# Kernel tuning notes

Measured on AMD Instinct MI355X. Metric: run time of the kernel, lower is better.

## Reference

```python
import jax, jax.numpy as jnp
import numpy as np

D_MODEL = 768
NHEAD = 12
DK = D_MODEL // NHEAD
MAX_DIST = 1000.0
FF = 3072
POS_HIDDEN = 32  # hidden width of the relative-position bias MLP
EPS = 1e-5
B, L = 2, 1024


def setup_inputs() -> dict:
    key = jax.random.key(0)
    ks = jax.random.split(key, 24)

    def lin(k, i, o):  # torch-Linear-like init, stored as (in, out)
        return jax.random.uniform(k, (i, o), jnp.float32, -1.0, 1.0) / np.sqrt(i)

    return {
        "src": jax.random.normal(ks[0], (B, L, D_MODEL), jnp.float32),
        "src_x": jax.random.uniform(ks[1], (B, L), jnp.float32) * 1000.0,
        "src_y": jax.random.uniform(ks[2], (B, L), jnp.float32) * 1000.0,
        # attention projections (q,k,v,out)
        "Wq": lin(ks[3], D_MODEL, D_MODEL), "bq": jnp.zeros((D_MODEL,), jnp.float32),
        "Wk": lin(ks[4], D_MODEL, D_MODEL), "bk": jnp.zeros((D_MODEL,), jnp.float32),
        "Wv": lin(ks[5], D_MODEL, D_MODEL), "bv": jnp.zeros((D_MODEL,), jnp.float32),
        "Wo": lin(ks[6], D_MODEL, D_MODEL), "bo": jnp.zeros((D_MODEL,), jnp.float32),
        # relative-position bias MLP: 2 -> POS_HIDDEN -> NHEAD
        "P1": lin(ks[7], 2, POS_HIDDEN), "pb1": jnp.zeros((POS_HIDDEN,), jnp.float32),
        "P2": lin(ks[8], POS_HIDDEN, NHEAD), "pb2": jnp.zeros((NHEAD,), jnp.float32),
        # FFN
        "W1": lin(ks[9], D_MODEL, FF), "b1": jnp.zeros((FF,), jnp.float32),
        "W2": lin(ks[10], FF, D_MODEL), "b2": jnp.zeros((D_MODEL,), jnp.float32),
        # post-LN params
        "g1": jnp.ones((D_MODEL,), jnp.float32), "be1": jnp.zeros((D_MODEL,), jnp.float32),
        "g2": jnp.ones((D_MODEL,), jnp.float32), "be2": jnp.zeros((D_MODEL,), jnp.float32),
    }


def _layernorm(x, g, b):
    m = jnp.mean(x, axis=-1, keepdims=True)
    v = jnp.var(x, axis=-1, keepdims=True)
    return (x - m) * jax.lax.rsqrt(v + EPS) * g + b


def reference(src, src_x, src_y, Wq, bq, Wk, bk, Wv, bv, Wo, bo,
              P1, pb1, P2, pb2, W1, b1, W2, b2, g1, be1, g2, be2):
    b, l, _ = src.shape
    # projections -> (b, h, l, dk)
    q = (src @ Wq + bq).reshape(b, l, NHEAD, DK).transpose(0, 2, 1, 3)
    k = (src @ Wk + bk).reshape(b, l, NHEAD, DK).transpose(0, 2, 1, 3)
    v = (src @ Wv + bv).reshape(b, l, NHEAD, DK).transpose(0, 2, 1, 3)
    # 2D relative positions, clipped and normalized to [-1, 1]
    rx = jnp.clip(src_x[:, :, None] - src_x[:, None, :], -MAX_DIST, MAX_DIST) / MAX_DIST
    ry = jnp.clip(src_y[:, :, None] - src_y[:, None, :], -MAX_DIST, MAX_DIST) / MAX_DIST
    rel = jnp.stack([rx, ry], axis=-1)                        # (b, l, l, 2)
    bias = jax.nn.relu(rel @ P1 + pb1) @ P2 + pb2             # (b, l, l, h)
    bias = bias.transpose(0, 3, 1, 2)                         # (b, h, l, l)
    scores = jnp.einsum('bhqd,bhkd->bhqk', q, k) / np.sqrt(DK).astype(np.float32) + bias
    attn = jax.nn.softmax(scores, axis=-1)
    o = jnp.einsum('bhqk,bhkd->bhqd', attn, v).transpose(0, 2, 1, 3).reshape(b, l, D_MODEL)
    src2 = o @ Wo + bo
    x = _layernorm(src + src2, g1, be1)                       # post-LN residual 1
    ff = jax.nn.relu(x @ W1 + b1) @ W2 + b2                   # FFN
    return _layernorm(x + ff, g2, be2)                        # post-LN residual 2
```

## Files before the change

kernel.cpp:

```cpp
#include <hip/hip_runtime.h>
#include <math.h>

typedef unsigned short ushort_t;
typedef __attribute__((ext_vector_type(8))) short bf16x8;
typedef __attribute__((ext_vector_type(4))) float f32x4;

constexpr int kD      = 768;
constexpr int kNH     = 12;
constexpr int kDK     = 64;
constexpr int kFF     = 3072;
constexpr int kL      = 1024;
constexpr int kRows   = 2048;
constexpr float kEPS  = 1e-5f;

__device__ __forceinline__ ushort_t f2bf(float f) {
    union { float f; unsigned u; } v; v.f = f;
    unsigned r = (v.u + 0x7fffu + ((v.u >> 16) & 1u)) >> 16;
    return (ushort_t)r;
}
__device__ __forceinline__ float bf2f(ushort_t u) {
    union { unsigned u; float f; } v; v.u = ((unsigned)u) << 16; return v.f;
}

#define GL_LDS(gp, lp) __builtin_amdgcn_global_load_lds( \
    (const __attribute__((address_space(1))) void*)(gp), \
    (__attribute__((address_space(3))) void*)(lp), 16, 0, 0)

template<int RELU, int OUTBF, int ADDBIAS>
__device__ __forceinline__ void gemm_body(const ushort_t* __restrict__ A,
                                          const ushort_t* __restrict__ WT,
                                          const float* __restrict__ bias,
                                          void* __restrict__ Cout,
                                          int N, int K, int row0, int col0,
                                          int kbeg, int kend)
{
    __shared__ ushort_t lds[8192];
    ushort_t* As = lds;
    ushort_t* Bs = lds + 4096;

    const int tid  = threadIdx.x;
    const int lane = tid & 63;
    const int wave = tid >> 6;
    const int wrow = (wave & 1) * 64;
    const int wcol = (wave >> 1) * 64;

    const int srow = wave * 16 + (lane >> 2);
    const int sk   = (lane & 3) * 8;
    const ushort_t* ga0 = A  + (size_t)(row0 + srow)      * K + sk;
    const ushort_t* ga1 = A  + (size_t)(row0 + srow + 64) * K + sk;
    const ushort_t* gb0 = WT + (size_t)(col0 + srow)      * K + sk;
    const ushort_t* gb1 = WT + (size_t)(col0 + srow + 64) * K + sk;
    ushort_t* la0 = As + wave * 512;
    ushort_t* la1 = As + 2048 + wave * 512;
    ushort_t* lb0 = Bs + wave * 512;
    ushort_t* lb1 = Bs + 2048 + wave * 512;

    const int fl = lane & 15, fq = lane >> 4;
    const ushort_t* fa[4];
    const ushort_t* fb[4];
    #pragma unroll
    for (int i = 0; i < 4; ++i) {
        fa[i] = As + (wrow + i * 16 + fl) * 32 + fq * 8;
        fb[i] = Bs + (wcol + i * 16 + fl) * 32 + fq * 8;
    }

    f32x4 acc[4][4] = {};

    for (int k0 = kbeg; k0 < kend; k0 += 32) {
        __syncthreads();
        GL_LDS(ga0 + k0, la0);
        GL_LDS(ga1 + k0, la1);
        GL_LDS(gb0 + k0, lb0);
        GL_LDS(gb1 + k0, lb1);
        __syncthreads();

        bf16x8 av[4], bv[4];
        #pragma unroll
        for (int i = 0; i < 4; ++i) {
            av[i] = *(const bf16x8*)fa[i];
            bv[i] = *(const bf16x8*)fb[i];
        }
        #pragma unroll
        for (int mi = 0; mi < 4; ++mi)
            #pragma unroll
            for (int ni = 0; ni < 4; ++ni)
                acc[mi][ni] = __builtin_amdgcn_mfma_f32_16x16x32_bf16(
                    av[mi], bv[ni], acc[mi][ni], 0, 0, 0);
    }

    #pragma unroll
    for (int mi = 0; mi < 4; ++mi) {
        const int m = wrow + mi * 16 + fq * 4;
        #pragma unroll
        for (int ni = 0; ni < 4; ++ni) {
            const int n = wcol + ni * 16 + fl;
            const float bb = ADDBIAS ? bias[col0 + n] : 0.f;
            #pragma unroll
            for (int r = 0; r < 4; ++r) {
                float v = acc[mi][ni][r] + bb;
                if (RELU) v = fmaxf(v, 0.f);
                const size_t idx = (size_t)(row0 + m + r) * N + col0 + n;
                if (OUTBF) ((ushort_t*)Cout)[idx] = f2bf(v);
                else       ((float*)Cout)[idx]    = v;
            }
        }
    }
}

template<int RELU, int OUTBF>
__global__ __launch_bounds__(256)
void gemm_kernel(const ushort_t* __restrict__ A, const ushort_t* __restrict__ WT,
                 const float* __restrict__ bias, void* __restrict__ Cout,
                 int N, int K)
{
    gemm_body<RELU, OUTBF, 1>(A, WT, bias, Cout, N, K,
                              blockIdx.y * 128, blockIdx.x * 128, 0, K);
}

__global__ __launch_bounds__(256)
void gemm_splitk_kernel(const ushort_t* __restrict__ A, const ushort_t* __restrict__ WT,
                        float* __restrict__ parts, int N, int K, int kslice)
{
    const int z = blockIdx.z;
    float* out = parts + (size_t)z * kRows * N;
    gemm_body<0, 0, 0>(A, WT, nullptr, out, N, K,
                       blockIdx.y * 128, blockIdx.x * 128, z * kslice, (z + 1) * kslice);
}

__global__ __launch_bounds__(256)
void gemm_qkv_kernel(const ushort_t* __restrict__ A,
                     const ushort_t* wq, const ushort_t* wk, const ushort_t* wv,
                     const float* bq, const float* bk, const float* bv,
                     ushort_t* q, ushort_t* k, ushort_t* v)
{
    const ushort_t* WT; const float* bias; ushort_t* out;
    if (blockIdx.z == 0)      { WT = wq; bias = bq; out = q; }
    else if (blockIdx.z == 1) { WT = wk; bias = bk; out = k; }
    else                      { WT = wv; bias = bv; out = v; }
    gemm_body<0, 1, 1>(A, WT, bias, out, kD, kD,
                       blockIdx.y * 128, blockIdx.x * 128, 0, kD);
}

struct WtDesc { const float* src; ushort_t* dst; int K; int N; };
struct WtArgs { WtDesc d[3]; };

__global__ __launch_bounds__(256)
void wt_kernel(WtArgs args)
{
    const WtDesc w = args.d[blockIdx.z];
    const int ktiles = w.K >> 6;
    const int kt = (blockIdx.x % ktiles) * 64;
    const int nt = (blockIdx.x / ktiles) * 64;
    if (nt >= w.N) return;

    __shared__ float T[64][65];
    const int tid = threadIdx.x;
    #pragma unroll
    for (int i = 0; i < 4; ++i) {
        const int e = tid + i * 256;
        const int r = e >> 4;
        const int c = (e & 15) * 4;
        const float4 f = *(const float4*)&w.src[(size_t)(kt + r) * w.N + nt + c];
        T[c + 0][r] = f.x; T[c + 1][r] = f.y; T[c + 2][r] = f.z; T[c + 3][r] = f.w;
    }
    __syncthreads();
    #pragma unroll
    for (int i = 0; i < 4; ++i) {
        const int e = tid + i * 256;
        const int n = e >> 4;
        const int kc = (e & 15) * 4;
        ushort4 o;
        o.x = f2bf(T[n][kc + 0]); o.y = f2bf(T[n][kc + 1]);
        o.z = f2bf(T[n][kc + 2]); o.w = f2bf(T[n][kc + 3]);
        *(ushort4*)&w.dst[(size_t)(nt + n) * w.K + kt + kc] = o;
    }
}

__global__ __launch_bounds__(256)
void cvt_kernel(const float* __restrict__ in, ushort_t* __restrict__ out, int n4)
{
    const int i = blockIdx.x * 256 + threadIdx.x;
    if (i < n4) {
        const float4 f = ((const float4*)in)[i];
        ushort4 o;
        o.x = f2bf(f.x); o.y = f2bf(f.y); o.z = f2bf(f.z); o.w = f2bf(f.w);
        ((ushort4*)out)[i] = o;
    }
}

__global__ __launch_bounds__(256)
void vtrans_kernel(const ushort_t* __restrict__ vb, ushort_t* __restrict__ vt)
{
    const int bh = blockIdx.x;
    const int b = bh / kNH, h = bh - b * kNH;
    const int j0 = blockIdx.y * 64;
    __shared__ ushort_t T[64][72];

    const int tid = threadIdx.x;
    {
        const int jr = tid & 63;
        const int c0 = (tid >> 6) * 16;
        const ushort_t* sp = vb + (size_t)(b * kL + j0 + jr) * kD + h * kDK + c0;
        uint4 u0 = *(const uint4*)sp;
        uint4 u1 = *(const uint4*)(sp + 8);
        const ushort_t* e0 = (const ushort_t*)&u0;
        const ushort_t* e1 = (const ushort_t*)&u1;
        #pragma unroll
        for (int jj = 0; jj < 8; ++jj) {
            T[c0 + jj][jr]     = e0[jj];
            T[c0 + 8 + jj][jr] = e1[jj];
        }
    }
    __syncthreads();
    {
        const int dr = tid >> 2;
        const int jc = (tid & 3) * 16;
        ushort_t* dp = vt + (size_t)(bh * 64 + dr) * kL + j0 + jc;
        *(uint4*)dp       = *(const uint4*)&T[dr][jc];
        *(uint4*)(dp + 8) = *(const uint4*)&T[dr][jc + 8];
    }
}

__global__ __launch_bounds__(256, 4)
void bias_kernel(const float* __restrict__ sx, const float* __restrict__ sy,
                 const float* __restrict__ P1, const float* __restrict__ pb1,
                 const float* __restrict__ P2, const float* __restrict__ pb2,
                 ushort_t* __restrict__ biasb)
{
    const int bid = blockIdx.x;
    const int b  = bid >> 10;
    const int qt = (bid >> 4) & 63;
    const int kt = bid & 15;
    const int tid = threadIdx.x;

    __shared__ float P[32][16];
    __shared__ float pb2l[12];
    __shared__ float qxl[16], qyl[16], kxl[64], kyl[64];
    __shared__ ushort_t Btile[12 * 1024];

    if (tid < 32) {
        P[tid][0] = P1[tid];
        P[tid][1] = P1[32 + tid];
        P[tid][2] = pb1[tid];
        P[tid][3] = 0.f;
    }
    for (int e = tid; e < 384; e += 256) P[e / 12][4 + e % 12] = P2[e];
    if (tid < 12) pb2l[tid] = pb2[tid];
    if (tid < 16) { qxl[tid] = sx[b * kL + qt * 16 + tid];
                    qyl[tid] = sy[b * kL + qt * 16 + tid]; }
    if (tid < 64) { kxl[tid] = sx[b * kL + kt * 64 + tid];
                    kyl[tid] = sy[b * kL + kt * 64 + tid]; }
    __syncthreads();

    const int ri = tid >> 4;
    const int fl = tid & 15;
    const int fq = ri >> 2, r = ri & 3;
    const int lane16 = fq * 16 + fl;
    const float xi = qxl[ri], yi = qyl[ri];

    float rx[4], ry[4];
    #pragma unroll
    for (int n = 0; n < 4; ++n) {
        const int cj = n * 16 + fl;
        rx[n] = fminf(fmaxf(xi - kxl[cj], -1000.f), 1000.f) * 1e-3f;
        ry[n] = fminf(fmaxf(yi - kyl[cj], -1000.f), 1000.f) * 1e-3f;
    }

    float acc[4][12] = {};
    #pragma unroll 4
    for (int u = 0; u < 32; ++u) {
        const float4 pc = *(const float4*)&P[u][0];
        const float4 w0 = *(const float4*)&P[u][4];
        const float4 w1 = *(const float4*)&P[u][8];
        const float4 w2 = *(const float4*)&P[u][12];
        float t[4];
        #pragma unroll
        for (int n = 0; n < 4; ++n)
            t[n] = fmaxf(fmaf(rx[n], pc.x, fmaf(ry[n], pc.y, pc.z)), 0.f);
        #pragma unroll
        for (int n = 0; n < 4; ++n) {
            acc[n][0]  = fmaf(t[n], w0.x, acc[n][0]);
            acc[n][1]  = fmaf(t[n], w0.y, acc[n][1]);
            acc[n][2]  = fmaf(t[n], w0.z, acc[n][2]);
            acc[n][3]  = fmaf(t[n], w0.w, acc[n][3]);
            acc[n][4]  = fmaf(t[n], w1.x, acc[n][4]);
            acc[n][5]  = fmaf(t[n], w1.y, acc[n][5]);
            acc[n][6]  = fmaf(t[n], w1.z, acc[n][6]);
            acc[n][7]  = fmaf(t[n], w1.w, acc[n][7]);
            acc[n][8]  = fmaf(t[n], w2.x, acc[n][8]);
            acc[n][9]  = fmaf(t[n], w2.y, acc[n][9]);
            acc[n][10] = fmaf(t[n], w2.z, acc[n][10]);
            acc[n][11] = fmaf(t[n], w2.w, acc[n][11]);
        }
    }

    #pragma unroll
    for (int h = 0; h < 12; ++h) {
        const float pb = pb2l[h] - 4.0f;
        #pragma unroll
        for (int n = 0; n < 4; ++n)
            Btile[h * 1024 + lane16 * 16 + n * 4 + r] = f2bf(acc[n][h] + pb);
    }
    __syncthreads();

    #pragma unroll
    for (int i = 0; i < 6; ++i) {
        const int off = (i * 256 + tid) * 8;
        const int h = off >> 10;
        const int inner = off & 1023;
        ushort_t* dst = biasb +
            (((size_t)(b * kNH + h) * 64 + qt) * 16 + kt) * 1024 + inner;
        *(uint4*)dst = *(const uint4*)&Btile[off];
    }
}

__global__ __launch_bounds__(256)
void attn_kernel(const ushort_t* __restrict__ qg, const ushort_t* __restrict__ kg,
                 const ushort_t* __restrict__ vt, const ushort_t* __restrict__ biasb,
                 ushort_t* __restrict__ og)
{
    const int bh = blockIdx.x;
    const int b  = bh / kNH, h = bh - b * kNH;
    const int qt = blockIdx.y;
    const int q0 = qt * 16;
    const int tid = threadIdx.x;
    const int z  = tid >> 6;
    const int lane = tid & 63;
    const int fl = lane & 15, fq = lane >> 4;

    __shared__ ushort_t Sp[4][16][72];
    __shared__ ushort_t Ob[4][16][64];
    __shared__ float    Ll[4][16];

    const size_t qoff = (size_t)(b * kL + q0 + fl) * kD + h * kDK + fq * 8;
    const bf16x8 aq0 = *(const bf16x8*)(qg + qoff);
    const bf16x8 aq1 = *(const bf16x8*)(qg + qoff + 32);

    const ushort_t* kbase = kg + (size_t)(b * kL) * kD + h * kDK + fq * 8;
    const ushort_t* vbase = vt + (size_t)(bh * 64) * kL + fq * 8;
    const ushort_t* btile = biasb +
        ((size_t)(bh * 64 + qt) * 16 + z * 4) * 1024 + lane * 16;

    f32x4 accO[4] = {};
    float l_part[4] = {};

    bf16x8 kc[4][2];
    uint4 bc0, bc1;
    {
        const int k0 = z * 256;
        #pragma unroll
        for (int n = 0; n < 4; ++n) {
            const ushort_t* kr = kbase + (size_t)(k0 + n * 16 + fl) * kD;
            kc[n][0] = *(const bf16x8*)kr;
            kc[n][1] = *(const bf16x8*)(kr + 32);
        }
        bc0 = *(const uint4*)btile;
        bc1 = *(const uint4*)(btile + 8);
    }

    #pragma unroll
    for (int t = 0; t < 4; ++t) {
        const int k0 = z * 256 + t * 64;

        bf16x8 vv[4][2];
        #pragma unroll
        for (int n = 0; n < 4; ++n) {
            const ushort_t* vr = vbase + (size_t)(n * 16 + fl) * kL + k0;
            vv[n][0] = *(const bf16x8*)vr;
            vv[n][1] = *(const bf16x8*)(vr + 32);
        }

        f32x4 S[4] = {};
        #pragma unroll
        for (int n = 0; n < 4; ++n) {
            S[n] = __builtin_amdgcn_mfma_f32_16x16x32_bf16(aq0, kc[n][0], S[n], 0, 0, 0);
            S[n] = __builtin_amdgcn_mfma_f32_16x16x32_bf16(aq1, kc[n][1], S[n], 0, 0, 0);
        }

        bf16x8 kn[4][2];
        uint4 bn0, bn1;
        if (t < 3) {
            #pragma unroll
            for (int n = 0; n < 4; ++n) {
                const ushort_t* kr = kbase + (size_t)(k0 + 64 + n * 16 + fl) * kD;
                kn[n][0] = *(const bf16x8*)kr;
                kn[n][1] = *(const bf16x8*)(kr + 32);
            }
            bn0 = *(const uint4*)(btile + (t + 1) * 1024);
            bn1 = *(const uint4*)(btile + (t + 1) * 1024 + 8);
        }

        ushort_t bu[16];
        *(uint4*)&bu[0] = bc0;
        *(uint4*)&bu[8] = bc1;

        #pragma unroll
        for (int n = 0; n < 4; ++n)
            #pragma unroll
            for (int r = 0; r < 4; ++r) {
                const float e = __expf(fmaf(S[n][r], 0.125f, bf2f(bu[n * 4 + r])));
                S[n][r] = e;
                l_part[r] += e;
            }

        #pragma unroll
        for (int n = 0; n < 4; ++n)
            #pragma unroll
            for (int r = 0; r < 4; ++r)
                Sp[z][fq * 4 + r][n * 16 + fl] = f2bf(S[n][r]);

        const bf16x8 ap0 = *(const bf16x8*)&Sp[z][fl][fq * 8];
        const bf16x8 ap1 = *(const bf16x8*)&Sp[z][fl][32 + fq * 8];
        #pragma unroll
        for (int n = 0; n < 4; ++n) {
            accO[n] = __builtin_amdgcn_mfma_f32_16x16x32_bf16(ap0, vv[n][0], accO[n], 0, 0, 0);
            accO[n] = __builtin_amdgcn_mfma_f32_16x16x32_bf16(ap1, vv[n][1], accO[n], 0, 0, 0);
        }

        if (t < 3) {
            #pragma unroll
            for (int n = 0; n < 4; ++n) { kc[n][0] = kn[n][0]; kc[n][1] = kn[n][1]; }
            bc0 = bn0; bc1 = bn1;
        }
    }

    float l_full[4], inv[4];
    #pragma unroll
    for (int r = 0; r < 4; ++r) {
        float l = l_part[r];
        l += __shfl_xor(l, 1, 16);
        l += __shfl_xor(l, 2, 16);
        l += __shfl_xor(l, 4, 16);
        l += __shfl_xor(l, 8, 16);
        l_full[r] = l;
        inv[r] = 1.0f / l;
    }

    #pragma unroll
    for (int n = 0; n < 4; ++n)
        #pragma unroll
        for (int r = 0; r < 4; ++r)
            Ob[z][fq * 4 + r][n * 16 + fl] = f2bf(accO[n][r] * inv[r]);
    if (fl == 0) {
        #pragma unroll
        for (int r = 0; r < 4; ++r)
            Ll[z][fq * 4 + r] = l_full[r];
    }
    __syncthreads();

    {
        const int ri = tid >> 4;
        const int d0 = (tid & 15) * 4;
        const float w0 = Ll[0][ri], w1 = Ll[1][ri], w2 = Ll[2][ri], w3 = Ll[3][ri];
        const float winv = 1.0f / (w0 + w1 + w2 + w3);
        const float c0 = w0 * winv, c1 = w1 * winv, c2 = w2 * winv, c3 = w3 * winv;

        ushort_t o[4];
        #pragma unroll
        for (int j = 0; j < 4; ++j)
            o[j] = f2bf(fmaf(c0, bf2f(Ob[0][ri][d0 + j]),
                        fmaf(c1, bf2f(Ob[1][ri][d0 + j]),
                        fmaf(c2, bf2f(Ob[2][ri][d0 + j]),
                             c3 * bf2f(Ob[3][ri][d0 + j])))));
        *(uint2*)&og[(size_t)(b * kL + q0 + ri) * kD + h * kDK + d0] = *(const uint2*)o;
    }
}

template<int NPART, int DUAL>
__global__ __launch_bounds__(256)
void ln_kernel(const float* __restrict__ a, const float* __restrict__ parts,
               const float* __restrict__ bias,
               const float* __restrict__ g, const float* __restrict__ be,
               float* __restrict__ out, ushort_t* __restrict__ out_bf)
{
    const int row = blockIdx.x;
    const int tid = threadIdx.x;
    const float* pa = a + (size_t)row * kD;
    constexpr size_t NTOK = (size_t)kRows * kD;

    float v[3];
    float s = 0.f, sq = 0.f;
    #pragma unroll
    for (int i = 0; i < 3; ++i) {
        const int d = tid + i * 256;
        float t = pa[d] + bias[d];
        #pragma unroll
        for (int p = 0; p < NPART; ++p)
            t += parts[p * NTOK + (size_t)row * kD + d];
        v[i] = t;
        s  += t;
        sq += t * t;
    }
    #pragma unroll
    for (int off = 32; off > 0; off >>= 1) {
        s  += __shfl_down(s, off);
        sq += __shfl_down(sq, off);
    }
    __shared__ float bs[4], bq2[4];
    if ((tid & 63) == 0) { bs[tid >> 6] = s; bq2[tid >> 6] = sq; }
    __syncthreads();
    const float ts = bs[0] + bs[1] + bs[2] + bs[3];
    const float tq = bq2[0] + bq2[1] + bq2[2] + bq2[3];
    const float invn = 1.0f / (float)kD;
    const float mean = ts * invn;
    const float var  = tq * invn - mean * mean;
    const float rstd = rsqrtf(var + kEPS);

    float* po = out + (size_t)row * kD;
    #pragma unroll
    for (int i = 0; i < 3; ++i) {
        const int d = tid + i * 256;
        const float o = (v[i] - mean) * rstd * g[d] + be[d];
        po[d] = o;
        if (DUAL) out_bf[(size_t)row * kD + d] = f2bf(o);
    }
}

extern "C" void kernel_launch(void* const* d_in, const int* in_sizes, int n_in,
                              void* d_out, int out_size, void* d_ws, size_t ws_size,
                              hipStream_t stream)
{
    const float* src = (const float*)d_in[0];
    const float* sx  = (const float*)d_in[1];
    const float* sy  = (const float*)d_in[2];
    const float* Wq  = (const float*)d_in[3];  const float* bq  = (const float*)d_in[4];
    const float* Wk  = (const float*)d_in[5];  const float* bk  = (const float*)d_in[6];
    const float* Wv  = (const float*)d_in[7];  const float* bv  = (const float*)d_in[8];
    const float* Wo  = (const float*)d_in[9];  const float* bo  = (const float*)d_in[10];
    const float* P1  = (const float*)d_in[11]; const float* pb1 = (const float*)d_in[12];
    const float* P2  = (const float*)d_in[13]; const float* pb2 = (const float*)d_in[14];
    const float* W1  = (const float*)d_in[15]; const float* b1  = (const float*)d_in[16];
    const float* W2  = (const float*)d_in[17]; const float* b2  = (const float*)d_in[18];
    const float* g1  = (const float*)d_in[19]; const float* be1 = (const float*)d_in[20];
    const float* g2  = (const float*)d_in[21]; const float* be2 = (const float*)d_in[22];

    constexpr size_t W768  = 768u * 768u;
    constexpr size_t W3072 = 768u * 3072u;
    constexpr size_t NTOK  = (size_t)kRows * kD;

    ushort_t* wsu = (ushort_t*)d_ws;
    ushort_t* wqT = wsu;
    ushort_t* wkT = wqT + W768;
    ushort_t* wvT = wkT + W768;
    ushort_t* qb  = wvT + W768;
    ushort_t* kb  = qb + NTOK;
    ushort_t* vb  = kb + NTOK;
    ushort_t* sb  = vb + NTOK;
    ushort_t* vtb = sb + NTOK;
    ushort_t* biasb = vtb + NTOK;
    ushort_t* woT   = biasb;
    ushort_t* w1T   = woT + W768;
    ushort_t* w2T   = w1T + W3072;
    float*    xb    = (float*)(w2T + W3072);
    ushort_t* h1bf  = (ushort_t*)(xb + NTOK);
    float*    s2p   = (float*)h1bf;
    float*    ff2p  = (float*)(h1bf + 4 * NTOK);
    ushort_t* xbf   = qb;

    const dim3 blk(256);

    WtArgs wa_early;
    wa_early.d[0] = { Wq, wqT, kD, kD };
    wa_early.d[1] = { Wk, wkT, kD, kD };
    wa_early.d[2] = { Wv, wvT, kD, kD };
    wt_kernel<<<dim3(144, 1, 3), blk, 0, stream>>>(wa_early);
    cvt_kernel<<<dim3((int)(NTOK / 4 / 256)), blk, 0, stream>>>(src, sb, (int)(NTOK / 4));
    bias_kernel<<<dim3(2048), blk, 0, stream>>>(sx, sy, P1, pb1, P2, pb2, biasb);

    gemm_qkv_kernel<<<dim3(kD / 128, kRows / 128, 3), blk, 0, stream>>>(
        sb, wqT, wkT, wvT, bq, bk, bv, qb, kb, vb);

    vtrans_kernel<<<dim3(2 * kNH, kL / 64), blk, 0, stream>>>(vb, vtb);

    attn_kernel<<<dim3(2 * kNH, kL / 16), blk, 0, stream>>>(qb, kb, vtb, biasb, sb);

    WtArgs wa_late;
    wa_late.d[0] = { Wo, woT, kD,  kD  };
    wa_late.d[1] = { W1, w1T, kD,  kFF };
    wa_late.d[2] = { W2, w2T, kFF, kD  };
    wt_kernel<<<dim3(576, 1, 3), blk, 0, stream>>>(wa_late);

    gemm_splitk_kernel<<<dim3(kD / 128, kRows / 128, 2), blk, 0, stream>>>(
        sb, woT, s2p, kD, kD, kD / 2);

    ln_kernel<2, 1><<<dim3(kRows), blk, 0, stream>>>(src, s2p, bo, g1, be1, xb, xbf);

    gemm_kernel<1, 1><<<dim3(kFF / 128, kRows / 128), blk, 0, stream>>>(
        xbf, w1T, b1, h1bf, kFF, kD);

    gemm_splitk_kernel<<<dim3(kD / 128, kRows / 128, 3), blk, 0, stream>>>(
        h1bf, w2T, ff2p, kD, kFF, kFF / 3);

    ln_kernel<3, 0><<<dim3(kRows), blk, 0, stream>>>(xb, ff2p, b2, g2, be2,
                                                     (float*)d_out, nullptr);
}
```

Measured before the change: 300.8 us.

## Merge independent kernels into combined launches to cut launch count and gaps

Three pairs of independent work now share one launch each, dispatched by block index: the Wq/Wk/Wv weight transposes with the src bf16 conversion, the QKV GEMM with the position-bias MLP, and attention with the late weight transposes (Wo/W1/W2). The late weight copies move to a separate buffer region after the FFN partial sums, since the old woT location overlaps the bias buffer that attention still reads. This removes three kernel launches and lets small jobs fill idle CUs beside heavier ones. In exchange, shared memory per block is sized to the largest branch, which can lower occupancy for the lighter branches, and block scheduling order affects how well the work overlaps.

Result: faster. 290.9 us (-3.3%).

```diff
diff --git a/kernel.cpp b/kernel.cpp
--- a/kernel.cpp
+++ b/kernel.cpp
@@ -32,9 +32,8 @@
                                           const float* __restrict__ bias,
                                           void* __restrict__ Cout,
                                           int N, int K, int row0, int col0,
-                                          int kbeg, int kend)
-{
-    __shared__ ushort_t lds[8192];
+                                          int kbeg, int kend, ushort_t* lds)
+{
     ushort_t* As = lds;
     ushort_t* Bs = lds + 4096;
 
@@ -113,54 +112,34 @@
                  const float* __restrict__ bias, void* __restrict__ Cout,
                  int N, int K)
 {
+    __shared__ ushort_t lds[8192];
     gemm_body<RELU, OUTBF, 1>(A, WT, bias, Cout, N, K,
-                              blockIdx.y * 128, blockIdx.x * 128, 0, K);
+                              blockIdx.y * 128, blockIdx.x * 128, 0, K, lds);
 }
 
 __global__ __launch_bounds__(256)
 void gemm_splitk_kernel(const ushort_t* __restrict__ A, const ushort_t* __restrict__ WT,
                         float* __restrict__ parts, int N, int K, int kslice)
 {
+    __shared__ ushort_t lds[8192];
     const int z = blockIdx.z;
     float* out = parts + (size_t)z * kRows * N;
     gemm_body<0, 0, 0>(A, WT, nullptr, out, N, K,
-                       blockIdx.y * 128, blockIdx.x * 128, z * kslice, (z + 1) * kslice);
-}
-
-__global__ __launch_bounds__(256)
-void gemm_qkv_kernel(const ushort_t* __restrict__ A,
-                     const ushort_t* wq, const ushort_t* wk, const ushort_t* wv,
-                     const float* bq, const float* bk, const float* bv,
-                     ushort_t* q, ushort_t* k, ushort_t* v)
-{
-    const ushort_t* WT; const float* bias; ushort_t* out;
-    if (blockIdx.z == 0)      { WT = wq; bias = bq; out = q; }
-    else if (blockIdx.z == 1) { WT = wk; bias = bk; out = k; }
-    else                      { WT = wv; bias = bv; out = v; }
-    gemm_body<0, 1, 1>(A, WT, bias, out, kD, kD,
-                       blockIdx.y * 128, blockIdx.x * 128, 0, kD);
-}
-
-struct WtDesc { const float* src; ushort_t* dst; int K; int N; };
-struct WtArgs { WtDesc d[3]; };
-
-__global__ __launch_bounds__(256)
-void wt_kernel(WtArgs args)
-{
-    const WtDesc w = args.d[blockIdx.z];
-    const int ktiles = w.K >> 6;
-    const int kt = (blockIdx.x % ktiles) * 64;
-    const int nt = (blockIdx.x / ktiles) * 64;
-    if (nt >= w.N) return;
-
-    __shared__ float T[64][65];
-    const int tid = threadIdx.x;
+                       blockIdx.y * 128, blockIdx.x * 128,
+                       z * kslice, (z + 1) * kslice, lds);
+}
+
+__device__ __forceinline__ void wt_tile(const float* __restrict__ src,
+                                        ushort_t* __restrict__ dst,
+                                        int K, int N, int kt, int nt,
+                                        float (*T)[65], int tid)
+{
     #pragma unroll
     for (int i = 0; i < 4; ++i) {
         const int e = tid + i * 256;
         const int r = e >> 4;
         const int c = (e & 15) * 4;
-        const float4 f = *(const float4*)&w.src[(size_t)(kt + r) * w.N + nt + c];
+        const float4 f = *(const float4*)&src[(size_t)(kt + r) * N + nt + c];
         T[c + 0][r] = f.x; T[c + 1][r] = f.y; T[c + 2][r] = f.z; T[c + 3][r] = f.w;
     }
     __syncthreads();
@@ -172,107 +151,92 @@
         ushort4 o;
         o.x = f2bf(T[n][kc + 0]); o.y = f2bf(T[n][kc + 1]);
         o.z = f2bf(T[n][kc + 2]); o.w = f2bf(T[n][kc + 3]);
-        *(ushort4*)&w.dst[(size_t)(nt + n) * w.K + kt + kc] = o;
+        *(ushort4*)&dst[(size_t)(nt + n) * K + kt + kc] = o;
     }
 }
 
 __global__ __launch_bounds__(256)
-void cvt_kernel(const float* __restrict__ in, ushort_t* __restrict__ out, int n4)
-{
-    const int i = blockIdx.x * 256 + threadIdx.x;
-    if (i < n4) {
-        const float4 f = ((const float4*)in)[i];
+void prep_kernel(const float* __restrict__ Wq, const float* __restrict__ Wk,
+                 const float* __restrict__ Wv,
+                 ushort_t* wqT, ushort_t* wkT, ushort_t* wvT,
+                 const float* __restrict__ src, ushort_t* __restrict__ sb)
+{
+    __shared__ float T[64][65];
+    const int bid = blockIdx.x;
+    const int tid = threadIdx.x;
+
+    if (bid < 432) {
+        const int wz = bid / 144, t = bid - wz * 144;
+        const float* s = (wz == 0) ? Wq : (wz == 1) ? Wk : Wv;
+        ushort_t*   d = (wz == 0) ? wqT : (wz == 1) ? wkT : wvT;
+        wt_tile(s, d, kD, kD, (t % 12) * 64, (t / 12) * 64, T, tid);
+    } else {
+        const int i = (bid - 432) * 256 + tid;
+        const float4 f = ((const float4*)src)[i];
         ushort4 o;
         o.x = f2bf(f.x); o.y = f2bf(f.y); o.z = f2bf(f.z); o.w = f2bf(f.w);
-        ((ushort4*)out)[i] = o;
-    }
-}
-
-__global__ __launch_bounds__(256)
-void vtrans_kernel(const ushort_t* __restrict__ vb, ushort_t* __restrict__ vt)
-{
-    const int bh = blockIdx.x;
-    const int b = bh / kNH, h = bh - b * kNH;
-    const int j0 = blockIdx.y * 64;
-    __shared__ ushort_t T[64][72];
-
-    const int tid = threadIdx.x;
-    {
-        const int jr = tid & 63;
-        const int c0 = (tid >> 6) * 16;
-        const ushort_t* sp = vb + (size_t)(b * kL + j0 + jr) * kD + h * kDK + c0;
-        uint4 u0 = *(const uint4*)sp;
-        uint4 u1 = *(const uint4*)(sp + 8);
-        const ushort_t* e0 = (const ushort_t*)&u0;
-        const ushort_t* e1 = (const ushort_t*)&u1;
-        #pragma unroll
-        for (int jj = 0; jj < 8; ++jj) {
-            T[c0 + jj][jr]     = e0[jj];
-            T[c0 + 8 + jj][jr] = e1[jj];
-        }
-    }
-    __syncthreads();
-    {
-        const int dr = tid >> 2;
-        const int jc = (tid & 3) * 16;
-        ushort_t* dp = vt + (size_t)(bh * 64 + dr) * kL + j0 + jc;
-        *(uint4*)dp       = *(const uint4*)&T[dr][jc];
-        *(uint4*)(dp + 8) = *(const uint4*)&T[dr][jc + 8];
-    }
-}
-
-__global__ __launch_bounds__(256, 4)
-void bias_kernel(const float* __restrict__ sx, const float* __restrict__ sy,
+        ((ushort4*)sb)[i] = o;
+    }
+}
+
+struct BiasSmem {
+    float P[32][16];
+    float pb2l[12];
+    float qxl[16], qyl[16], kxl[64], kyl[64];
+    ushort_t Btile[12 * 1024];
+};
+struct AttnSmem {
+    ushort_t Sp[4][16][72];
+    ushort_t Ob[4][16][64];
+    float    Ll[4][16];
+};
+
+__device__ __forceinline__ void bias_body(int bid, BiasSmem& S,
+                 const float* __restrict__ sx, const float* __restrict__ sy,
                  const float* __restrict__ P1, const float* __restrict__ pb1,
                  const float* __restrict__ P2, const float* __restrict__ pb2,
                  ushort_t* __restrict__ biasb)
 {
-    const int bid = blockIdx.x;
     const int b  = bid >> 10;
     const int qt = (bid >> 4) & 63;
     const int kt = bid & 15;
     const int tid = threadIdx.x;
 
-    __shared__ float P[32][16];
-    __shared__ float pb2l[12];
-    __shared__ float qxl[16], qyl[16], kxl[64], kyl[64];
-    __shared__ ushort_t Btile[12 * 1024];
-
     if (tid < 32) {
-        P[tid][0] = P1[tid];
-        P[tid][1] = P1[32 + tid];
-        P[tid][2] = pb1[tid];
-        P[tid][3] = 0.f;
-    }
-    for (int e = tid; e < 384; e += 256) P[e / 12][4 + e % 12] = P2[e];
-    if (tid < 12) pb2l[tid] = pb2[tid];
-    if (tid < 16) { qxl[tid] = sx[b * kL + qt * 16 + tid];
-                    qyl[tid] = sy[b * kL + qt * 16 + tid]; }
-    if (tid < 64) { kxl[tid] = sx[b * kL + kt * 64 + tid];
-                    kyl[tid] = sy[b * kL + kt * 64 + tid]; }
+        S.P[tid][0] = P1[tid];
+        S.P[tid][1] = P1[32 + tid];
+        S.P[tid][2] = pb1[tid];
+        S.P[tid][3] = 0.f;
+    }
+    for (int e = tid; e < 384; e += 256) S.P[e / 12][4 + e % 12] = P2[e];
+    if (tid < 12) S.pb2l[tid] = pb2[tid];
+    if (tid < 16) { S.qxl[tid] = sx[b * kL + qt * 16 + tid];
+                    S.qyl[tid] = sy[b * kL + qt * 16 + tid]; }
+    if (tid < 64) { S.kxl[tid] = sx[b * kL + kt * 64 + tid];
+                    S.kyl[tid] = sy[b * kL + kt * 64 + tid]; }
     __syncthreads();
 
     const int ri = tid >> 4;
     const int fl = tid & 15;
     const int fq = ri >> 2, r = ri & 3;
     const int lane16 = fq * 16 + fl;
-    const float xi = qxl[ri], yi = qyl[ri];
+    const float xi = S.qxl[ri], yi = S.qyl[ri];
 
     float rx[4], ry[4];
     #pragma unroll
     for (int n = 0; n < 4; ++n) {
         const int cj = n * 16 + fl;
-        rx[n] = fminf(fmaxf(xi - kxl[cj], -1000.f), 1000.f) * 1e-3f;
-        ry[n] = fminf(fmaxf(yi - kyl[cj], -1000.f), 1000.f) * 1e-3f;
+        rx[n] = fminf(fmaxf(xi - S.kxl[cj], -1000.f), 1000.f) * 1e-3f;
+        ry[n] = fminf(fmaxf(yi - S.kyl[cj], -1000.f), 1000.f) * 1e-3f;
     }
 
     float acc[4][12] = {};
     #pragma unroll 4
     for (int u = 0; u < 32; ++u) {
-        const float4 pc = *(const float4*)&P[u][0];
-        const float4 w0 = *(const float4*)&P[u][4];
-        const float4 w1 = *(const float4*)&P[u][8];
-        const float4 w2 = *(const float4*)&P[u][12];
+        const float4 pc = *(const float4*)&S.P[u][0];
+        const float4 w0 = *(const float4*)&S.P[u][4];
+        const float4 w1 = *(const float4*)&S.P[u][8];
+        const float4 w2 = *(const float4*)&S.P[u][12];
         float t[4];
         #pragma unroll
         for (int n = 0; n < 4; ++n)
@@ -296,10 +260,10 @@
 
     #pragma unroll
     for (int h = 0; h < 12; ++h) {
-        const float pb = pb2l[h] - 4.0f;
+        const float pb = S.pb2l[h] - 4.0f;
         #pragma unroll
         for (int n = 0; n < 4; ++n)
-            Btile[h * 1024 + lane16 * 16 + n * 4 + r] = f2bf(acc[n][h] + pb);
+            S.Btile[h * 1024 + lane16 * 16 + n * 4 + r] = f2bf(acc[n][h] + pb);
     }
     __syncthreads();
 
@@ -310,27 +274,105 @@
         const int inner = off & 1023;
         ushort_t* dst = biasb +
             (((size_t)(b * kNH + h) * 64 + qt) * 16 + kt) * 1024 + inner;
-        *(uint4*)dst = *(const uint4*)&Btile[off];
+        *(uint4*)dst = *(const uint4*)&S.Btile[off];
     }
 }
 
 __global__ __launch_bounds__(256)
-void attn_kernel(const ushort_t* __restrict__ qg, const ushort_t* __restrict__ kg,
-                 const ushort_t* __restrict__ vt, const ushort_t* __restrict__ biasb,
-                 ushort_t* __restrict__ og)
+void qkv_bias_kernel(const ushort_t* __restrict__ A,
+                     const ushort_t* wq, const ushort_t* wk, const ushort_t* wv,
+                     const float* bq, const float* bk, const float* bv,
+                     ushort_t* q, ushort_t* k, ushort_t* v,
+                     const float* __restrict__ sx, const float* __restrict__ sy,
+                     const float* __restrict__ P1, const float* __restrict__ pb1,
+                     const float* __restrict__ P2, const float* __restrict__ pb2,
+                     ushort_t* __restrict__ biasb)
+{
+    __shared__ __align__(16) char smem[sizeof(BiasSmem)];
+    const int bid = blockIdx.x;
+
+    if (bid < 288) {
+        const int z = bid / 96, rem = bid - z * 96;
+        const int bx = rem % 6, by = rem / 6;
+        const ushort_t* WT; const float* bias; ushort_t* out;
+        if (z == 0)      { WT = wq; bias = bq; out = q; }
+        else if (z == 1) { WT = wk; bias = bk; out = k; }
+        else             { WT = wv; bias = bv; out = v; }
+        gemm_body<0, 1, 1>(A, WT, bias, out, kD, kD,
+                           by * 128, bx * 128, 0, kD, (ushort_t*)smem);
+    } else {
+        bias_body(bid - 288, *(BiasSmem*)smem, sx, sy, P1, pb1, P2, pb2, biasb);
+    }
+}
+
+__global__ __launch_bounds__(256)
+void vtrans_kernel(const ushort_t* __restrict__ vb, ushort_t* __restrict__ vt)
 {
     const int bh = blockIdx.x;
+    const int b = bh / kNH, h = bh - b * kNH;
+    const int j0 = blockIdx.y * 64;
+    __shared__ ushort_t T[64][72];
+
+    const int tid = threadIdx.x;
+    {
+        const int jr = tid & 63;
+        const int c0 = (tid >> 6) * 16;
+        const ushort_t* sp = vb + (size_t)(b * kL + j0 + jr) * kD + h * kDK + c0;
+        uint4 u0 = *(const uint4*)sp;
+        uint4 u1 = *(const uint4*)(sp + 8);
+        const ushort_t* e0 = (const ushort_t*)&u0;
+        const ushort_t* e1 = (const ushort_t*)&u1;
+        #pragma unroll
+        for (int jj = 0; jj < 8; ++jj) {
+            T[c0 + jj][jr]     = e0[jj];
+            T[c0 + 8 + jj][jr] = e1[jj];
+        }
+    }
+    __syncthreads();
+    {
+        const int dr = tid >> 2;
+        const int jc = (tid & 3) * 16;
+        ushort_t* dp = vt + (size_t)(bh * 64 + dr) * kL + j0 + jc;
+        *(uint4*)dp       = *(const uint4*)&T[dr][jc];
+        *(uint4*)(dp + 8) = *(const uint4*)&T[dr][jc + 8];
+    }
+}
+
+constexpr size_t kAttnWtSmem =
+    sizeof(AttnSmem) > sizeof(float) * 64 * 65 ? sizeof(AttnSmem)
+                                               : sizeof(float) * 64 * 65;
+
+__global__ __launch_bounds__(256)
+void attn_wt_kernel(const ushort_t* __restrict__ qg, const ushort_t* __restrict__ kg,
+                    const ushort_t* __restrict__ vt, const ushort_t* __restrict__ biasb,
+                    ushort_t* __restrict__ og,
+                    const float* __restrict__ Wo, const float* __restrict__ W1,
+                    const float* __restrict__ W2,
+                    ushort_t* woT, ushort_t* w1T, ushort_t* w2T)
+{
+    __shared__ __align__(16) char smem[kAttnWtSmem];
+    const int bid = blockIdx.x;
+    const int tid = threadIdx.x;
+
+    if (bid >= 1536) {
+        float (*T)[65] = (float(*)[65])smem;
+        const int t = bid - 1536;
+        if (t < 144)      wt_tile(Wo, woT, kD,  kD,  (t % 12) * 64, (t / 12) * 64, T, tid);
+        else if (t < 720) { const int t2 = t - 144;
+                            wt_tile(W1, w1T, kD,  kFF, (t2 % 12) * 64, (t2 / 12) * 64, T, tid); }
+        else              { const int t2 = t - 720;
+                            wt_tile(W2, w2T, kFF, kD,  (t2 % 48) * 64, (t2 / 48) * 64, T, tid); }
+        return;
+    }
+
+    AttnSmem& S = *(AttnSmem*)smem;
+    const int bh = bid >> 6;
+    const int qt = bid & 63;
     const int b  = bh / kNH, h = bh - b * kNH;
-    const int qt = blockIdx.y;
     const int q0 = qt * 16;
-    const int tid = threadIdx.x;
     const int z  = tid >> 6;
     const int lane = tid & 63;
     const int fl = lane & 15, fq = lane >> 4;
-
-    __shared__ ushort_t Sp[4][16][72];
-    __shared__ ushort_t Ob[4][16][64];
-    __shared__ float    Ll[4][16];
 
     const size_t qoff = (size_t)(b * kL + q0 + fl) * kD + h * kDK + fq * 8;
     const bf16x8 aq0 = *(const bf16x8*)(qg + qoff);
@@ -370,11 +412,11 @@
             vv[n][1] = *(const bf16x8*)(vr + 32);
         }
 
-        f32x4 S[4] = {};
+        f32x4 Sv[4] = {};
         #pragma unroll
         for (int n = 0; n < 4; ++n) {
-            S[n] = __builtin_amdgcn_mfma_f32_16x16x32_bf16(aq0, kc[n][0], S[n], 0, 0, 0);
-            S[n] = __builtin_amdgcn_mfma_f32_16x16x32_bf16(aq1, kc[n][1], S[n], 0, 0, 0);
+            Sv[n] = __builtin_amdgcn_mfma_f32_16x16x32_bf16(aq0, kc[n][0], Sv[n], 0, 0, 0);
+            Sv[n] = __builtin_amdgcn_mfma_f32_16x16x32_bf16(aq1, kc[n][1], Sv[n], 0, 0, 0);
         }
 
         bf16x8 kn[4][2];
@@ -398,8 +440,8 @@
         for (int n = 0; n < 4; ++n)
             #pragma unroll
             for (int r = 0; r < 4; ++r) {
-                const float e = __expf(fmaf(S[n][r], 0.125f, bf2f(bu[n * 4 + r])));
-                S[n][r] = e;
+                const float e = __expf(fmaf(Sv[n][r], 0.125f, bf2f(bu[n * 4 + r])));
+                Sv[n][r] = e;
                 l_part[r] += e;
             }
 
@@ -407,10 +449,10 @@
         for (int n = 0; n < 4; ++n)
             #pragma unroll
             for (int r = 0; r < 4; ++r)
-                Sp[z][fq * 4 + r][n * 16 + fl] = f2bf(S[n][r]);
-
-        const bf16x8 ap0 = *(const bf16x8*)&Sp[z][fl][fq * 8];
-        const bf16x8 ap1 = *(const bf16x8*)&Sp[z][fl][32 + fq * 8];
+                S.Sp[z][fq * 4 + r][n * 16 + fl] = f2bf(Sv[n][r]);
+
+        const bf16x8 ap0 = *(const bf16x8*)&S.Sp[z][fl][fq * 8];
+        const bf16x8 ap1 = *(const bf16x8*)&S.Sp[z][fl][32 + fq * 8];
         #pragma unroll
         for (int n = 0; n < 4; ++n) {
             accO[n] = __builtin_amdgcn_mfma_f32_16x16x32_bf16(ap0, vv[n][0], accO[n], 0, 0, 0);
@@ -440,28 +482,28 @@
     for (int n = 0; n < 4; ++n)
         #pragma unroll
         for (int r = 0; r < 4; ++r)
-            Ob[z][fq * 4 + r][n * 16 + fl] = f2bf(accO[n][r] * inv[r]);
+            S.Ob[z][fq * 4 + r][n * 16 + fl] = f2bf(accO[n][r] * inv[r]);
     if (fl == 0) {
         #pragma unroll
         for (int r = 0; r < 4; ++r)
-            Ll[z][fq * 4 + r] = l_full[r];
+            S.Ll[z][fq * 4 + r] = l_full[r];
     }
     __syncthreads();
 
     {
         const int ri = tid >> 4;
         const int d0 = (tid & 15) * 4;
-        const float w0 = Ll[0][ri], w1 = Ll[1][ri], w2 = Ll[2][ri], w3 = Ll[3][ri];
+        const float w0 = S.Ll[0][ri], w1 = S.Ll[1][ri], w2 = S.Ll[2][ri], w3 = S.Ll[3][ri];
         const float winv = 1.0f / (w0 + w1 + w2 + w3);
         const float c0 = w0 * winv, c1 = w1 * winv, c2 = w2 * winv, c3 = w3 * winv;
 
         ushort_t o[4];
         #pragma unroll
         for (int j = 0; j < 4; ++j)
-            o[j] = f2bf(fmaf(c0, bf2f(Ob[0][ri][d0 + j]),
-                        fmaf(c1, bf2f(Ob[1][ri][d0 + j]),
-                        fmaf(c2, bf2f(Ob[2][ri][d0 + j]),
-                             c3 * bf2f(Ob[3][ri][d0 + j])))));
+            o[j] = f2bf(fmaf(c0, bf2f(S.Ob[0][ri][d0 + j]),
+                        fmaf(c1, bf2f(S.Ob[1][ri][d0 + j]),
+                        fmaf(c2, bf2f(S.Ob[2][ri][d0 + j]),
+                             c3 * bf2f(S.Ob[3][ri][d0 + j])))));
         *(uint2*)&og[(size_t)(b * kL + q0 + ri) * kD + h * kDK + d0] = *(const uint2*)o;
     }
 }
@@ -559,37 +601,34 @@
 
     const dim3 blk(256);
 
-    WtArgs wa_early;
-    wa_early.d[0] = { Wq, wqT, kD, kD };
-    wa_early.d[1] = { Wk, wkT, kD, kD };
-    wa_early.d[2] = { Wv, wvT, kD, kD };
-    wt_kernel<<<dim3(144, 1, 3), blk, 0, stream>>>(wa_early);
-    cvt_kernel<<<dim3((int)(NTOK / 4 / 256)), blk, 0, stream>>>(src, sb, (int)(NTOK / 4));
-    bias_kernel<<<dim3(2048), blk, 0, stream>>>(sx, sy, P1, pb1, P2, pb2, biasb);
-
-    gemm_qkv_kernel<<<dim3(kD / 128, kRows / 128, 3), blk, 0, stream>>>(
-        sb, wqT, wkT, wvT, bq, bk, bv, qb, kb, vb);
+    prep_kernel<<<dim3(1968), blk, 0, stream>>>(Wq, Wk, Wv, wqT, wkT, wvT, src, sb);
+
+    qkv_bias_kernel<<<dim3(2336), blk, 0, stream>>>(
+        sb, wqT, wkT, wvT, bq, bk, bv, qb, kb, vb,
+        sx, sy, P1, pb1, P2, pb2, biasb);
 
     vtrans_kernel<<<dim3(2 * kNH, kL / 64), blk, 0, stream>>>(vb, vtb);
 
-    attn_kernel<<<dim3(2 * kNH, kL / 16), blk, 0, stream>>>(qb, kb, vtb, biasb, sb);
-
-    WtArgs wa_late;
-    wa_late.d[0] = { Wo, woT, kD,  kD  };
-    wa_late.d[1] = { W1, w1T, kD,  kFF };
-    wa_late.d[2] = { W2, w2T, kFF, kD  };
-    wt_kernel<<<dim3(576, 1, 3), blk, 0, stream>>>(wa_late);
+    attn_wt_kernel<<<dim3(2832), blk, 0, stream>>>(
+        qb, kb, vtb, biasb, sb, Wo, W1, W2,
+        (ushort_t*)(ff2p + 3 * NTOK),
+        (ushort_t*)(ff2p + 3 * NTOK) + W768,
+        (ushort_t*)(ff2p + 3 * NTOK) + W768 + W3072);
+
+    ushort_t* woT2 = (ushort_t*)(ff2p + 3 * NTOK);
+    ushort_t* w1T2 = woT2 + W768;
+    ushort_t* w2T2 = w1T2 + W3072;
 
     gemm_splitk_kernel<<<dim3(kD / 128, kRows / 128, 2), blk, 0, stream>>>(
-        sb, woT, s2p, kD, kD, kD / 2);
+        sb, woT2, s2p, kD, kD, kD / 2);
 
     ln_kernel<2, 1><<<dim3(kRows), blk, 0, stream>>>(src, s2p, bo, g1, be1, xb, xbf);
 
     gemm_kernel<1, 1><<<dim3(kFF / 128, kRows / 128), blk, 0, stream>>>(
-        xbf, w1T, b1, h1bf, kFF, kD);
+        xbf, w1T2, b1, h1bf, kFF, kD);
 
     gemm_splitk_kernel<<<dim3(kD / 128, kRows / 128, 3), blk, 0, stream>>>(
-        h1bf, w2T, ff2p, kD, kFF, kFF / 3);
+        h1bf, w2T2, ff2p, kD, kFF, kFF / 3);
 
     ln_kernel<3, 0><<<dim3(kRows), blk, 0, stream>>>(xb, ff2p, b2, g2, be2,
                                                      (float*)d_out, nullptr);
```
